# Kernel optimization log

Hardware: AMD Instinct MI355X
Metric: run time of the kernel (lower is better)

The kernel has to match this reference:

```python
import jax, jax.numpy as jnp
import numpy as np

B, N, IN_DIM, HEADS, PER_HEAD = 8, 512, 256, 4, 32
OUT_DIM = HEADS * PER_HEAD  # 128
NEG_SLOPE = 0.2


def setup_inputs() -> dict:
    key = jax.random.key(0)
    ks = jax.random.split(key, 8)
    x = jax.random.normal(ks[0], (B, N, IN_DIM), jnp.float32)
    adj = jax.random.randint(ks[1], (B, N, N), 0, 2, jnp.int32)
    sl = 1.0 / np.sqrt(IN_DIM)
    W_l = jax.random.normal(ks[2], (IN_DIM, OUT_DIM), jnp.float32) * sl  # source proj
    b_l = jnp.zeros((OUT_DIM,), jnp.float32)
    W_r = jax.random.normal(ks[3], (IN_DIM, OUT_DIM), jnp.float32) * sl  # target proj
    b_r = jnp.zeros((OUT_DIM,), jnp.float32)
    att = jax.random.normal(ks[4], (HEADS, PER_HEAD), jnp.float32) * (1.0 / np.sqrt(PER_HEAD))
    bias = jnp.zeros((OUT_DIM,), jnp.float32)
    return {"x": x, "adj": adj, "W_l": W_l, "b_l": b_l, "W_r": W_r, "b_r": b_r,
            "att": att, "bias": bias}


def _gatv2_single(x_b, adj_b, W_l, b_l, W_r, b_r, att, bias):
    # PyG GATv2Conv: remove_self_loops + add_self_loops -> diagonal forced to 1
    n = x_b.shape[0]
    adj_sl = jnp.fill_diagonal(adj_b, 1, inplace=False)
    # edge_index = adj.nonzero().t(): source = row, target = col
    m = (adj_sl != 0).T  # m[i, j]: source j feeds target i
    xl = (x_b @ W_l + b_l).reshape(n, HEADS, PER_HEAD)  # source-side features
    xr = (x_b @ W_r + b_r).reshape(n, HEADS, PER_HEAD)  # target-side features
    s = xr[:, None] + xl[None, :]                       # [i, j, H, C]
    s = jnp.where(s > 0, s, NEG_SLOPE * s)              # LeakyReLU(0.2)
    e = jnp.einsum('ijhc,hc->ijh', s, att)              # attention logits
    e = jnp.where(m[..., None], e, -jnp.inf)
    alpha = jax.nn.softmax(e, axis=1)                   # softmax over sources j
    out = jnp.einsum('ijh,jhc->ihc', alpha, xl).reshape(n, HEADS * PER_HEAD)
    return out + bias


def reference(x, adj, W_l, b_l, W_r, b_r, att, bias):
    # Sequential per-batch processing, faithful to the original Python loop
    # and keeping the [N,N,H,C] intermediate to one graph at a time.
    def one(args):
        x_b, adj_b = args
        return _gatv2_single(x_b, adj_b, W_l, b_l, W_r, b_r, att, bias)
    return jax.lax.map(one, (x, adj))  # [B, N, OUT_DIM]
```

## Files before the change

kernel.cpp:

```cpp
#include <hip/hip_runtime.h>

#define B_   8
#define N_   512
#define IND  256
#define H_   4
#define PH   32
#define OD   128
#define TI   2

typedef float v2f __attribute__((ext_vector_type(2)));

#define ATT_SCALE 0.5770780163555854f
#define DLR_SCALE 0.8656170245333781f

template <int PAT>
__device__ __forceinline__ float dpp_add(float x) {
    int yi = __builtin_amdgcn_mov_dpp(__float_as_int(x), PAT, 0xF, 0xF, true);
    return x + __int_as_float(yi);
}

__device__ __forceinline__ float fast_exp2(float x) {
#if __has_builtin(__builtin_amdgcn_exp2f)
    return __builtin_amdgcn_exp2f(x);
#else
    return exp2f(x);
#endif
}

__device__ __forceinline__ void pk_fma(v2f& d, v2f a, v2f b) {
    asm("v_pk_fma_f32 %0, %1, %2, %0" : "+v"(d) : "v"(a), "v"(b));
}

__global__ __launch_bounds__(512, 2) void proj_kernel(
    const float* __restrict__ x,
    const float* __restrict__ Wl, const float* __restrict__ bl,
    const float* __restrict__ Wr, const float* __restrict__ br,
    const float* __restrict__ att,
    float* __restrict__ xl, float* __restrict__ xr,
    float* __restrict__ dl, float* __restrict__ dr)
{
    __shared__ float xs[8 * IND];
    __shared__ float comb[3][128][17];

    const int t = threadIdx.x;
    const int row0 = blockIdx.x * 8;

    ((float4*)xs)[t] = ((const float4*)(x + (size_t)row0 * IND))[t];
    __syncthreads();

    const int og    = t & 31;
    const int rr    = (t >> 5) & 1;
    const int ks    = (t >> 6) & 3;
    const int which = t >> 8;
    const int o0 = og * 4;
    const int r0 = rr * 4;
    const int k0 = ks * 64;
    const float* W = (which ? Wr : Wl) + (size_t)k0 * OD + o0;

    float acc[4][4];
    #pragma unroll
    for (int r = 0; r < 4; ++r)
        #pragma unroll
        for (int c = 0; c < 4; ++c) acc[r][c] = 0.f;

    float4 wb[2][4];
    #pragma unroll
    for (int kk = 0; kk < 4; ++kk)
        wb[0][kk] = *(const float4*)(W + (size_t)kk * OD);

    #pragma unroll 2
    for (int s = 0; s < 16; ++s) {
        const int cur = s & 1, nxt = cur ^ 1;
        if (s < 15) {
            const float* Wq = W + (size_t)((s + 1) * 4) * OD;
            #pragma unroll
            for (int kk = 0; kk < 4; ++kk)
                wb[nxt][kk] = *(const float4*)(Wq + (size_t)kk * OD);
        }
        float xv[4][4];
        #pragma unroll
        for (int r = 0; r < 4; ++r)
            *(float4*)(xv[r]) = *(const float4*)(&xs[(r0 + r) * IND + k0 + s * 4]);
        #pragma unroll
        for (int kk = 0; kk < 4; ++kk)
            #pragma unroll
            for (int r = 0; r < 4; ++r) {
                acc[r][0] = fmaf(xv[r][kk], wb[cur][kk].x, acc[r][0]);
                acc[r][1] = fmaf(xv[r][kk], wb[cur][kk].y, acc[r][1]);
                acc[r][2] = fmaf(xv[r][kk], wb[cur][kk].z, acc[r][2]);
                acc[r][3] = fmaf(xv[r][kk], wb[cur][kk].w, acc[r][3]);
            }
    }

    const int pid = og | (rr << 5) | (which << 6);
    if (ks != 0) {
        #pragma unroll
        for (int i = 0; i < 16; ++i)
            comb[ks - 1][pid][i] = acc[i >> 2][i & 3];
    }
    __syncthreads();
    if (ks == 0) {
        const float* bb = which ? br : bl;
        float* dst = which ? xr : xl;
        float* dp  = which ? dr : dl;
        float4 bv = *(const float4*)(bb + o0);
        float4 av = *(const float4*)(att + o0);
        const float bvf[4] = {bv.x, bv.y, bv.z, bv.w};
        const float avf[4] = {av.x, av.y, av.z, av.w};
        #pragma unroll
        for (int r = 0; r < 4; ++r) {
            float y[4];
            #pragma unroll
            for (int c = 0; c < 4; ++c)
                y[c] = ((acc[r][c] + comb[0][pid][r * 4 + c])
                      + (comb[1][pid][r * 4 + c] + comb[2][pid][r * 4 + c]))
                      + bvf[c];
            *(float4*)(&dst[(size_t)(row0 + r0 + r) * OD + o0]) =
                make_float4(y[0], y[1], y[2], y[3]);
            float dc = fmaf(avf[0], y[0], fmaf(avf[1], y[1],
                       fmaf(avf[2], y[2], avf[3] * y[3])));
            dc += __shfl_xor(dc, 1);
            dc += __shfl_xor(dc, 2);
            dc += __shfl_xor(dc, 4);
            if ((og & 7) == 0)
                dp[(size_t)(row0 + r0 + r) * H_ + (og >> 3)] = DLR_SCALE * dc;
        }
    }
}

__global__ __launch_bounds__(256, 3) void attn_kernel(
    const int* __restrict__ adj, const float* __restrict__ att,
    const float* __restrict__ bias,
    const float* __restrict__ xl, const float* __restrict__ xr,
    const float* __restrict__ dl, const float* __restrict__ dr,
    float* __restrict__ out)
{
    __shared__ float sacc[H_][TI][16][PH + 1];
    __shared__ float ssum[H_][16][TI];

    const int t = threadIdx.x;
    const int bid = (blockIdx.x & 7) * 256 + (blockIdx.x >> 3);
    const int b  = bid >> 8;
    const int i0 = (bid & 255) * TI;
    const int cq = t & 3;
    const int js = (t >> 2) & 15;
    const int h  = t >> 6;
    const int cbase = h * PH + cq * 8;

    float atS[8];
    {
        const float* ap = att + cbase;
        float4 a0 = *(const float4*)(ap);
        float4 a1 = *(const float4*)(ap + 4);
        atS[0] = ATT_SCALE * a0.x; atS[1] = ATT_SCALE * a0.y;
        atS[2] = ATT_SCALE * a0.z; atS[3] = ATT_SCALE * a0.w;
        atS[4] = ATT_SCALE * a1.x; atS[5] = ATT_SCALE * a1.y;
        atS[6] = ATT_SCALE * a1.z; atS[7] = ATT_SCALE * a1.w;
    }
    float xrS[TI][8];
    float drv[TI];
    #pragma unroll
    for (int il = 0; il < TI; ++il) {
        const float* xp = xr + ((size_t)(b * N_ + i0 + il)) * OD + cbase;
        float4 r0 = *(const float4*)(xp);
        float4 r1 = *(const float4*)(xp + 4);
        xrS[il][0] = r0.x; xrS[il][1] = r0.y; xrS[il][2] = r0.z; xrS[il][3] = r0.w;
        xrS[il][4] = r1.x; xrS[il][5] = r1.y; xrS[il][6] = r1.z; xrS[il][7] = r1.w;
        drv[il] = dr[((size_t)(b * N_ + i0 + il)) * H_ + h];
    }

    v2f acc[TI][4];
    float sumw[TI];
    #pragma unroll
    for (int il = 0; il < TI; ++il) {
        sumw[il] = 0.f;
        #pragma unroll
        for (int m = 0; m < 4; ++m) acc[il][m] = (v2f){0.f, 0.f};
    }

    const float* xlp = xl + ((size_t)(b * N_ + js)) * OD + cbase;
    const int*   ajp = adj + ((size_t)(b * N_ + js)) * N_ + i0;
    const float* dlp = dl + ((size_t)(b * N_ + js)) * H_ + h;

    float4 va = *(const float4*)(xlp);
    float4 vb = *(const float4*)(xlp + 4);
    int2   mj = *(const int2*)(ajp);
    float  dj = *dlp;

    #pragma unroll 2
    for (int u = 0; u < 32; ++u) {
        float4 wa = va, wb = vb;
        int2   wm = mj;
        float  wd = dj;
        if (u < 31) {
            xlp += 16 * OD; ajp += 16 * N_; dlp += 16 * H_;
            va = *(const float4*)(xlp);
            vb = *(const float4*)(xlp + 4);
            mj = *(const int2*)(ajp);
            dj = *dlp;
        }
        const int j = u * 16 + js;
        v2f p0 = (v2f){wa.x, wa.y}, p1 = (v2f){wa.z, wa.w};
        v2f p2 = (v2f){wb.x, wb.y}, p3 = (v2f){wb.z, wb.w};
        int wmv[TI] = {wm.x, wm.y};
        #pragma unroll
        for (int il = 0; il < TI; ++il) {
            float s, e2a = 0.f, e2b = 0.f;
            s = xrS[il][0] + wa.x; e2a = fmaf(atS[0], __builtin_fabsf(s), e2a);
            s = xrS[il][1] + wa.y; e2b = fmaf(atS[1], __builtin_fabsf(s), e2b);
            s = xrS[il][2] + wa.z; e2a = fmaf(atS[2], __builtin_fabsf(s), e2a);
            s = xrS[il][3] + wa.w; e2b = fmaf(atS[3], __builtin_fabsf(s), e2b);
            s = xrS[il][4] + wb.x; e2a = fmaf(atS[4], __builtin_fabsf(s), e2a);
            s = xrS[il][5] + wb.y; e2b = fmaf(atS[5], __builtin_fabsf(s), e2b);
            s = xrS[il][6] + wb.z; e2a = fmaf(atS[6], __builtin_fabsf(s), e2a);
            s = xrS[il][7] + wb.w; e2b = fmaf(atS[7], __builtin_fabsf(s), e2b);
            float eh = e2a + e2b;
            eh = dpp_add<0xB1>(eh);
            eh = dpp_add<0x4E>(eh);
            float e = (wd + drv[il]) + eh;
            bool keep = (wmv[il] != 0) || (j == i0 + il);
            float w = keep ? fast_exp2(e) : 0.f;
            sumw[il] += w;
            v2f ws = (v2f){w, w};
            pk_fma(acc[il][0], ws, p0);
            pk_fma(acc[il][1], ws, p1);
            pk_fma(acc[il][2], ws, p2);
            pk_fma(acc[il][3], ws, p3);
        }
    }

    #pragma unroll
    for (int il = 0; il < TI; ++il) {
        float4 w0 = make_float4(acc[il][0].x, acc[il][0].y,
                                acc[il][1].x, acc[il][1].y);
        float4 w1 = make_float4(acc[il][2].x, acc[il][2].y,
                                acc[il][3].x, acc[il][3].y);
        *(float4*)(&sacc[h][il][js][cq * 8])     = w0;
        *(float4*)(&sacc[h][il][js][cq * 8 + 4]) = w1;
    }
    if (cq == 0) {
        #pragma unroll
        for (int il = 0; il < TI; ++il)
            ssum[h][js][il] = sumw[il];
    }
    __syncthreads();

    const int lane = t & 63;
    const int il2  = lane >> 5;
    const int c    = lane & 31;
    float st = 0.f;
    #pragma unroll
    for (int k = 0; k < 16; ++k) st += ssum[h][k][il2];
    float a = 0.f;
    #pragma unroll
    for (int k = 0; k < 16; ++k) a += sacc[h][il2][k][c];
    const float inv = 1.f / st;
    const int cg = h * PH + c;
    out[((size_t)(b * N_ + i0 + il2)) * OD + cg] = fmaf(a, inv, bias[cg]);
}

extern "C" void kernel_launch(void* const* d_in, const int* in_sizes, int n_in,
                              void* d_out, int out_size, void* d_ws, size_t ws_size,
                              hipStream_t stream) {
    const float* x    = (const float*)d_in[0];
    const int*   adj  = (const int*)d_in[1];
    const float* Wl   = (const float*)d_in[2];
    const float* bl   = (const float*)d_in[3];
    const float* Wr   = (const float*)d_in[4];
    const float* br   = (const float*)d_in[5];
    const float* att  = (const float*)d_in[6];
    const float* bias = (const float*)d_in[7];
    float* out = (float*)d_out;

    float* xl = (float*)d_ws;
    float* xr = xl + (size_t)B_ * N_ * OD;
    float* dl = xr + (size_t)B_ * N_ * OD;
    float* dr = dl + (size_t)B_ * N_ * H_;

    proj_kernel<<<512, 512, 0, stream>>>(x, Wl, bl, Wr, br, att, xl, xr, dl, dr);
    attn_kernel<<<2048, 256, 0, stream>>>(adj, att, bias, xl, xr, dl, dr, out);
}
```

Baseline: 123.6 us.

## Double attention target tile and rebalance projection kernel across more threads

The attention kernel now processes four target rows per block instead of two. Each loaded source feature row and its int4 adjacency load are therefore reused across more targets, and the grid is halved. The projection kernel moves to 1024 threads, each computing 2 rows instead of 4, and drops the register double-buffering of W loads in favour of a simple unrolled loop. The final reduction writes float2 outputs. Higher per-thread register pressure in attn (TI=4) may reduce occupancy, and 1024-thread launch bounds could limit registers in proj.

```diff
diff --git a/kernel.cpp b/kernel.cpp
--- a/kernel.cpp
+++ b/kernel.cpp
@@ -6,7 +6,7 @@
 #define H_   4
 #define PH   32
 #define OD   128
-#define TI   2
+#define TI   4
 
 typedef float v2f __attribute__((ext_vector_type(2)));
 
@@ -31,7 +31,7 @@
     asm("v_pk_fma_f32 %0, %1, %2, %0" : "+v"(d) : "v"(a), "v"(b));
 }
 
-__global__ __launch_bounds__(512, 2) void proj_kernel(
+__global__ __launch_bounds__(1024, 4) void proj_kernel(
     const float* __restrict__ x,
     const float* __restrict__ Wl, const float* __restrict__ bl,
     const float* __restrict__ Wr, const float* __restrict__ br,
@@ -40,62 +40,60 @@
     float* __restrict__ dl, float* __restrict__ dr)
 {
     __shared__ float xs[8 * IND];
-    __shared__ float comb[3][128][17];
+    __shared__ float comb[3][256][9];
 
     const int t = threadIdx.x;
     const int row0 = blockIdx.x * 8;
 
-    ((float4*)xs)[t] = ((const float4*)(x + (size_t)row0 * IND))[t];
+    if (t < 512)
+        ((float4*)xs)[t] = ((const float4*)(x + (size_t)row0 * IND))[t];
     __syncthreads();
 
     const int og    = t & 31;
-    const int rr    = (t >> 5) & 1;
-    const int ks    = (t >> 6) & 3;
-    const int which = t >> 8;
+    const int rh    = (t >> 5) & 3;
+    const int ks    = (t >> 7) & 3;
+    const int which = t >> 9;
     const int o0 = og * 4;
-    const int r0 = rr * 4;
+    const int r0 = rh * 2;
     const int k0 = ks * 64;
     const float* W = (which ? Wr : Wl) + (size_t)k0 * OD + o0;
-
-    float acc[4][4];
-    #pragma unroll
-    for (int r = 0; r < 4; ++r)
+    const float* xsa = &xs[r0 * IND + k0];
+    const float* xsb = &xs[(r0 + 1) * IND + k0];
+
+    float acc[2][4];
+    #pragma unroll
+    for (int r = 0; r < 2; ++r)
         #pragma unroll
         for (int c = 0; c < 4; ++c) acc[r][c] = 0.f;
 
-    float4 wb[2][4];
-    #pragma unroll
-    for (int kk = 0; kk < 4; ++kk)
-        wb[0][kk] = *(const float4*)(W + (size_t)kk * OD);
-
-    #pragma unroll 2
-    for (int s = 0; s < 16; ++s) {
-        const int cur = s & 1, nxt = cur ^ 1;
-        if (s < 15) {
-            const float* Wq = W + (size_t)((s + 1) * 4) * OD;
-            #pragma unroll
-            for (int kk = 0; kk < 4; ++kk)
-                wb[nxt][kk] = *(const float4*)(Wq + (size_t)kk * OD);
-        }
-        float xv[4][4];
-        #pragma unroll
-        for (int r = 0; r < 4; ++r)
-            *(float4*)(xv[r]) = *(const float4*)(&xs[(r0 + r) * IND + k0 + s * 4]);
-        #pragma unroll
-        for (int kk = 0; kk < 4; ++kk)
-            #pragma unroll
-            for (int r = 0; r < 4; ++r) {
-                acc[r][0] = fmaf(xv[r][kk], wb[cur][kk].x, acc[r][0]);
-                acc[r][1] = fmaf(xv[r][kk], wb[cur][kk].y, acc[r][1]);
-                acc[r][2] = fmaf(xv[r][kk], wb[cur][kk].z, acc[r][2]);
-                acc[r][3] = fmaf(xv[r][kk], wb[cur][kk].w, acc[r][3]);
-            }
-    }
-
-    const int pid = og | (rr << 5) | (which << 6);
+    #pragma unroll 4
+    for (int s = 0; s < 32; ++s) {
+        float4 w0 = *(const float4*)(W + (size_t)(2 * s) * OD);
+        float4 w1 = *(const float4*)(W + (size_t)(2 * s + 1) * OD);
+        float2 xa = *(const float2*)(xsa + 2 * s);
+        float2 xb = *(const float2*)(xsb + 2 * s);
+        acc[0][0] = fmaf(xa.x, w0.x, acc[0][0]);
+        acc[0][1] = fmaf(xa.x, w0.y, acc[0][1]);
+        acc[0][2] = fmaf(xa.x, w0.z, acc[0][2]);
+        acc[0][3] = fmaf(xa.x, w0.w, acc[0][3]);
+        acc[1][0] = fmaf(xb.x, w0.x, acc[1][0]);
+        acc[1][1] = fmaf(xb.x, w0.y, acc[1][1]);
+        acc[1][2] = fmaf(xb.x, w0.z, acc[1][2]);
+        acc[1][3] = fmaf(xb.x, w0.w, acc[1][3]);
+        acc[0][0] = fmaf(xa.y, w1.x, acc[0][0]);
+        acc[0][1] = fmaf(xa.y, w1.y, acc[0][1]);
+        acc[0][2] = fmaf(xa.y, w1.z, acc[0][2]);
+        acc[0][3] = fmaf(xa.y, w1.w, acc[0][3]);
+        acc[1][0] = fmaf(xb.y, w1.x, acc[1][0]);
+        acc[1][1] = fmaf(xb.y, w1.y, acc[1][1]);
+        acc[1][2] = fmaf(xb.y, w1.z, acc[1][2]);
+        acc[1][3] = fmaf(xb.y, w1.w, acc[1][3]);
+    }
+
+    const int pid = og | (rh << 5) | (which << 7);
     if (ks != 0) {
         #pragma unroll
-        for (int i = 0; i < 16; ++i)
+        for (int i = 0; i < 8; ++i)
             comb[ks - 1][pid][i] = acc[i >> 2][i & 3];
     }
     __syncthreads();
@@ -108,7 +106,7 @@
         const float bvf[4] = {bv.x, bv.y, bv.z, bv.w};
         const float avf[4] = {av.x, av.y, av.z, av.w};
         #pragma unroll
-        for (int r = 0; r < 4; ++r) {
+        for (int r = 0; r < 2; ++r) {
             float y[4];
             #pragma unroll
             for (int c = 0; c < 4; ++c)
@@ -139,9 +137,9 @@
     __shared__ float ssum[H_][16][TI];
 
     const int t = threadIdx.x;
-    const int bid = (blockIdx.x & 7) * 256 + (blockIdx.x >> 3);
-    const int b  = bid >> 8;
-    const int i0 = (bid & 255) * TI;
+    const int bid = (blockIdx.x & 7) * 128 + (blockIdx.x >> 3);
+    const int b  = bid >> 7;
+    const int i0 = (bid & 127) * TI;
     const int cq = t & 3;
     const int js = (t >> 2) & 15;
     const int h  = t >> 6;
@@ -184,25 +182,25 @@
 
     float4 va = *(const float4*)(xlp);
     float4 vb = *(const float4*)(xlp + 4);
-    int2   mj = *(const int2*)(ajp);
+    int4   mj = *(const int4*)(ajp);
     float  dj = *dlp;
 
     #pragma unroll 2
     for (int u = 0; u < 32; ++u) {
         float4 wa = va, wb = vb;
-        int2   wm = mj;
+        int4   wm = mj;
         float  wd = dj;
         if (u < 31) {
             xlp += 16 * OD; ajp += 16 * N_; dlp += 16 * H_;
             va = *(const float4*)(xlp);
             vb = *(const float4*)(xlp + 4);
-            mj = *(const int2*)(ajp);
+            mj = *(const int4*)(ajp);
             dj = *dlp;
         }
         const int j = u * 16 + js;
         v2f p0 = (v2f){wa.x, wa.y}, p1 = (v2f){wa.z, wa.w};
         v2f p2 = (v2f){wb.x, wb.y}, p3 = (v2f){wb.z, wb.w};
-        int wmv[TI] = {wm.x, wm.y};
+        int wmv[TI] = {wm.x, wm.y, wm.z, wm.w};
         #pragma unroll
         for (int il = 0; il < TI; ++il) {
             float s, e2a = 0.f, e2b = 0.f;
@@ -246,17 +244,23 @@
     __syncthreads();
 
     const int lane = t & 63;
-    const int il2  = lane >> 5;
-    const int c    = lane & 31;
+    const int o = lane * 2;
+    const int il2 = o >> 5;
+    const int c2 = o & 31;
     float st = 0.f;
     #pragma unroll
     for (int k = 0; k < 16; ++k) st += ssum[h][k][il2];
-    float a = 0.f;
-    #pragma unroll
-    for (int k = 0; k < 16; ++k) a += sacc[h][il2][k][c];
+    float a0 = 0.f, a1 = 0.f;
+    #pragma unroll
+    for (int k = 0; k < 16; ++k) {
+        float2 p = *(const float2*)(&sacc[h][il2][k][c2]);
+        a0 += p.x; a1 += p.y;
+    }
     const float inv = 1.f / st;
-    const int cg = h * PH + c;
-    out[((size_t)(b * N_ + i0 + il2)) * OD + cg] = fmaf(a, inv, bias[cg]);
+    const int c = h * PH + c2;
+    float* op = out + ((size_t)(b * N_ + i0 + il2)) * OD;
+    *(float2*)(&op[c]) = make_float2(fmaf(a0, inv, bias[c]),
+                                     fmaf(a1, inv, bias[c + 1]));
 }
 
 extern "C" void kernel_launch(void* const* d_in, const int* in_sizes, int n_in,
@@ -277,6 +281,6 @@
     float* dl = xr + (size_t)B_ * N_ * OD;
     float* dr = dl + (size_t)B_ * N_ * H_;
 
-    proj_kernel<<<512, 512, 0, stream>>>(x, Wl, bl, Wr, br, att, xl, xr, dl, dr);
-    attn_kernel<<<2048, 256, 0, stream>>>(adj, att, bias, xl, xr, dl, dr, out);
-}
+    proj_kernel<<<512, 1024, 0, stream>>>(x, Wl, bl, Wr, br, att, xl, xr, dl, dr);
+    attn_kernel<<<1024, 256, 0, stream>>>(adj, att, bias, xl, xr, dl, dr, out);
+}
```

Result: slower. 126.4 us (+2.3%).

## Widen target tile to four rows and reduce attention partials with shuffles

Applied to the files above, without the earlier changes.

The attention kernel now handles four target rows per block (half as many blocks), so each loaded source feature row, mask int4 and logit term is reused across more targets. The register prefetch is dropped in favour of direct loads. The shared-memory reduction is replaced by xor-shuffle butterfly reductions across the 16 source lanes. The projection kernel is re-split so each thread covers all 8 rows over a 32-wide K slice, with an 8-way shared-memory combine done by all threads. Register pressure rises with TI=4 while the launch bound asks for 4 blocks per SM, and losing the prefetch may expose load latency.

```diff
diff --git a/kernel.cpp b/kernel.cpp
--- a/kernel.cpp
+++ b/kernel.cpp
@@ -6,7 +6,7 @@
 #define H_   4
 #define PH   32
 #define OD   128
-#define TI   2
+#define TI   4
 
 typedef float v2f __attribute__((ext_vector_type(2)));
 
@@ -40,7 +40,7 @@
     float* __restrict__ dl, float* __restrict__ dr)
 {
     __shared__ float xs[8 * IND];
-    __shared__ float comb[3][128][17];
+    __shared__ float comb[8][64][33];
 
     const int t = threadIdx.x;
     const int row0 = blockIdx.x * 8;
@@ -49,17 +49,15 @@
     __syncthreads();
 
     const int og    = t & 31;
-    const int rr    = (t >> 5) & 1;
-    const int ks    = (t >> 6) & 3;
+    const int ks    = (t >> 5) & 7;
     const int which = t >> 8;
     const int o0 = og * 4;
-    const int r0 = rr * 4;
-    const int k0 = ks * 64;
+    const int k0 = ks * 32;
     const float* W = (which ? Wr : Wl) + (size_t)k0 * OD + o0;
 
-    float acc[4][4];
-    #pragma unroll
-    for (int r = 0; r < 4; ++r)
+    float acc[8][4];
+    #pragma unroll
+    for (int r = 0; r < 8; ++r)
         #pragma unroll
         for (int c = 0; c < 4; ++c) acc[r][c] = 0.f;
 
@@ -69,82 +67,84 @@
         wb[0][kk] = *(const float4*)(W + (size_t)kk * OD);
 
     #pragma unroll 2
-    for (int s = 0; s < 16; ++s) {
+    for (int s = 0; s < 8; ++s) {
         const int cur = s & 1, nxt = cur ^ 1;
-        if (s < 15) {
+        if (s < 7) {
             const float* Wq = W + (size_t)((s + 1) * 4) * OD;
             #pragma unroll
             for (int kk = 0; kk < 4; ++kk)
                 wb[nxt][kk] = *(const float4*)(Wq + (size_t)kk * OD);
         }
-        float xv[4][4];
-        #pragma unroll
-        for (int r = 0; r < 4; ++r)
-            *(float4*)(xv[r]) = *(const float4*)(&xs[(r0 + r) * IND + k0 + s * 4]);
-        #pragma unroll
-        for (int kk = 0; kk < 4; ++kk)
+        float4 xv[8];
+        #pragma unroll
+        for (int r = 0; r < 8; ++r)
+            xv[r] = *(const float4*)(&xs[r * IND + k0 + s * 4]);
+        #pragma unroll
+        for (int kk = 0; kk < 4; ++kk) {
             #pragma unroll
-            for (int r = 0; r < 4; ++r) {
-                acc[r][0] = fmaf(xv[r][kk], wb[cur][kk].x, acc[r][0]);
-                acc[r][1] = fmaf(xv[r][kk], wb[cur][kk].y, acc[r][1]);
-                acc[r][2] = fmaf(xv[r][kk], wb[cur][kk].z, acc[r][2]);
-                acc[r][3] = fmaf(xv[r][kk], wb[cur][kk].w, acc[r][3]);
+            for (int r = 0; r < 8; ++r) {
+                const float xk = (kk == 0) ? xv[r].x : (kk == 1) ? xv[r].y
+                               : (kk == 2) ? xv[r].z : xv[r].w;
+                acc[r][0] = fmaf(xk, wb[cur][kk].x, acc[r][0]);
+                acc[r][1] = fmaf(xk, wb[cur][kk].y, acc[r][1]);
+                acc[r][2] = fmaf(xk, wb[cur][kk].z, acc[r][2]);
+                acc[r][3] = fmaf(xk, wb[cur][kk].w, acc[r][3]);
             }
-    }
-
-    const int pid = og | (rr << 5) | (which << 6);
-    if (ks != 0) {
-        #pragma unroll
-        for (int i = 0; i < 16; ++i)
-            comb[ks - 1][pid][i] = acc[i >> 2][i & 3];
-    }
+        }
+    }
+
+    const int pid = og | (which << 5);
+    #pragma unroll
+    for (int i = 0; i < 32; ++i)
+        comb[ks][pid][i] = acc[i >> 2][i & 3];
     __syncthreads();
-    if (ks == 0) {
-        const float* bb = which ? br : bl;
-        float* dst = which ? xr : xl;
-        float* dp  = which ? dr : dl;
-        float4 bv = *(const float4*)(bb + o0);
-        float4 av = *(const float4*)(att + o0);
-        const float bvf[4] = {bv.x, bv.y, bv.z, bv.w};
-        const float avf[4] = {av.x, av.y, av.z, av.w};
-        #pragma unroll
-        for (int r = 0; r < 4; ++r) {
-            float y[4];
-            #pragma unroll
-            for (int c = 0; c < 4; ++c)
-                y[c] = ((acc[r][c] + comb[0][pid][r * 4 + c])
-                      + (comb[1][pid][r * 4 + c] + comb[2][pid][r * 4 + c]))
-                      + bvf[c];
-            *(float4*)(&dst[(size_t)(row0 + r0 + r) * OD + o0]) =
-                make_float4(y[0], y[1], y[2], y[3]);
-            float dc = fmaf(avf[0], y[0], fmaf(avf[1], y[1],
-                       fmaf(avf[2], y[2], avf[3] * y[3])));
-            dc += __shfl_xor(dc, 1);
-            dc += __shfl_xor(dc, 2);
-            dc += __shfl_xor(dc, 4);
-            if ((og & 7) == 0)
-                dp[(size_t)(row0 + r0 + r) * H_ + (og >> 3)] = DLR_SCALE * dc;
-        }
-    }
-}
-
-__global__ __launch_bounds__(256, 3) void attn_kernel(
+
+    const int ogf = t & 31;
+    const int rf  = (t >> 5) & 7;
+    const int whf = t >> 8;
+    const int pidf = ogf | (whf << 5);
+    const float* bb = whf ? br : bl;
+    float* dst = whf ? xr : xl;
+    float* dp  = whf ? dr : dl;
+    float4 bv = *(const float4*)(bb + ogf * 4);
+    float4 av = *(const float4*)(att + ogf * 4);
+    const float bvf[4] = {bv.x, bv.y, bv.z, bv.w};
+    const float avf[4] = {av.x, av.y, av.z, av.w};
+    float y[4];
+    #pragma unroll
+    for (int c = 0; c < 4; ++c) {
+        const int idx = rf * 4 + c;
+        float s01 = comb[0][pidf][idx] + comb[1][pidf][idx];
+        float s23 = comb[2][pidf][idx] + comb[3][pidf][idx];
+        float s45 = comb[4][pidf][idx] + comb[5][pidf][idx];
+        float s67 = comb[6][pidf][idx] + comb[7][pidf][idx];
+        y[c] = ((s01 + s23) + (s45 + s67)) + bvf[c];
+    }
+    *(float4*)(&dst[(size_t)(row0 + rf) * OD + ogf * 4]) =
+        make_float4(y[0], y[1], y[2], y[3]);
+    float dc = fmaf(avf[0], y[0], fmaf(avf[1], y[1],
+               fmaf(avf[2], y[2], avf[3] * y[3])));
+    dc += __shfl_xor(dc, 1);
+    dc += __shfl_xor(dc, 2);
+    dc += __shfl_xor(dc, 4);
+    if ((ogf & 7) == 0)
+        dp[(size_t)(row0 + rf) * H_ + (ogf >> 3)] = DLR_SCALE * dc;
+}
+
+__global__ __launch_bounds__(256, 4) void attn_kernel(
     const int* __restrict__ adj, const float* __restrict__ att,
     const float* __restrict__ bias,
     const float* __restrict__ xl, const float* __restrict__ xr,
     const float* __restrict__ dl, const float* __restrict__ dr,
     float* __restrict__ out)
 {
-    __shared__ float sacc[H_][TI][16][PH + 1];
-    __shared__ float ssum[H_][16][TI];
-
     const int t = threadIdx.x;
-    const int bid = (blockIdx.x & 7) * 256 + (blockIdx.x >> 3);
-    const int b  = bid >> 8;
-    const int i0 = (bid & 255) * TI;
+    const int bid = (blockIdx.x & 7) * 128 + (blockIdx.x >> 3);
+    const int b  = bid >> 7;
+    const int i0 = (bid & 127) * TI;
     const int cq = t & 3;
+    const int h  = t >> 6;
     const int js = (t >> 2) & 15;
-    const int h  = t >> 6;
     const int cbase = h * PH + cq * 8;
 
     float atS[8];
@@ -182,27 +182,18 @@
     const int*   ajp = adj + ((size_t)(b * N_ + js)) * N_ + i0;
     const float* dlp = dl + ((size_t)(b * N_ + js)) * H_ + h;
 
-    float4 va = *(const float4*)(xlp);
-    float4 vb = *(const float4*)(xlp + 4);
-    int2   mj = *(const int2*)(ajp);
-    float  dj = *dlp;
-
     #pragma unroll 2
     for (int u = 0; u < 32; ++u) {
-        float4 wa = va, wb = vb;
-        int2   wm = mj;
-        float  wd = dj;
-        if (u < 31) {
-            xlp += 16 * OD; ajp += 16 * N_; dlp += 16 * H_;
-            va = *(const float4*)(xlp);
-            vb = *(const float4*)(xlp + 4);
-            mj = *(const int2*)(ajp);
-            dj = *dlp;
-        }
+        float4 wa = *(const float4*)(xlp);
+        float4 wb = *(const float4*)(xlp + 4);
+        int4   wm = *(const int4*)(ajp);
+        float  wd = *dlp;
+        xlp += 16 * OD; ajp += 16 * N_; dlp += 16 * H_;
+
         const int j = u * 16 + js;
         v2f p0 = (v2f){wa.x, wa.y}, p1 = (v2f){wa.z, wa.w};
         v2f p2 = (v2f){wb.x, wb.y}, p3 = (v2f){wb.z, wb.w};
-        int wmv[TI] = {wm.x, wm.y};
+        int wmv[TI] = {wm.x, wm.y, wm.z, wm.w};
         #pragma unroll
         for (int il = 0; il < TI; ++il) {
             float s, e2a = 0.f, e2b = 0.f;
@@ -230,33 +221,32 @@
     }
 
     #pragma unroll
-    for (int il = 0; il < TI; ++il) {
-        float4 w0 = make_float4(acc[il][0].x, acc[il][0].y,
-                                acc[il][1].x, acc[il][1].y);
-        float4 w1 = make_float4(acc[il][2].x, acc[il][2].y,
-                                acc[il][3].x, acc[il][3].y);
-        *(float4*)(&sacc[h][il][js][cq * 8])     = w0;
-        *(float4*)(&sacc[h][il][js][cq * 8 + 4]) = w1;
-    }
-    if (cq == 0) {
-        #pragma unroll
-        for (int il = 0; il < TI; ++il)
-            ssum[h][js][il] = sumw[il];
-    }
-    __syncthreads();
-
-    const int lane = t & 63;
-    const int il2  = lane >> 5;
-    const int c    = lane & 31;
-    float st = 0.f;
-    #pragma unroll
-    for (int k = 0; k < 16; ++k) st += ssum[h][k][il2];
-    float a = 0.f;
-    #pragma unroll
-    for (int k = 0; k < 16; ++k) a += sacc[h][il2][k][c];
-    const float inv = 1.f / st;
-    const int cg = h * PH + c;
-    out[((size_t)(b * N_ + i0 + il2)) * OD + cg] = fmaf(a, inv, bias[cg]);
+    for (int m = 4; m <= 32; m <<= 1) {
+        #pragma unroll
+        for (int il = 0; il < TI; ++il) {
+            sumw[il] += __shfl_xor(sumw[il], m);
+            #pragma unroll
+            for (int q = 0; q < 4; ++q) {
+                acc[il][q].x += __shfl_xor(acc[il][q].x, m);
+                acc[il][q].y += __shfl_xor(acc[il][q].y, m);
+            }
+        }
+    }
+
+    const int g = js;
+    if (g < 8) {
+        const int il  = g >> 1;
+        const int hf  = g & 1;
+        const float inv = 1.f / sumw[il];
+        const int c0 = cbase + hf * 4;
+        float4 bq = *(const float4*)(bias + c0);
+        v2f a0 = acc[il][2 * hf], a1 = acc[il][2 * hf + 1];
+        float4 vout = make_float4(fmaf(a0.x, inv, bq.x),
+                                  fmaf(a0.y, inv, bq.y),
+                                  fmaf(a1.x, inv, bq.z),
+                                  fmaf(a1.y, inv, bq.w));
+        *(float4*)(&out[((size_t)(b * N_ + i0 + il)) * OD + c0]) = vout;
+    }
 }
 
 extern "C" void kernel_launch(void* const* d_in, const int* in_sizes, int n_in,
@@ -278,5 +268,5 @@
     float* dr = dl + (size_t)B_ * N_ * H_;
 
     proj_kernel<<<512, 512, 0, stream>>>(x, Wl, bl, Wr, br, att, xl, xr, dl, dr);
-    attn_kernel<<<2048, 256, 0, stream>>>(adj, att, bias, xl, xr, dl, dr, out);
-}
+    attn_kernel<<<1024, 256, 0, stream>>>(adj, att, bias, xl, xr, dl, dr, out);
+}
```

After: 127.8 us. +3.4%, slower.
